# Performance work log

Measured on AMD Instinct MI355X. Metric: run time of the kernel, lower is better.

The kernel has to match this reference:

```python
import jax, jax.numpy as jnp
import numpy as np

EMBED_DIM = 1024
NUM_HEADS = 16
HEAD_DIM = EMBED_DIM // NUM_HEADS
SCALE = 1.0 / float(np.sqrt(HEAD_DIM))


def setup_inputs() -> dict:
    key = jax.random.key(0)
    ks = jax.random.split(key, 5)
    B, S, E = 2, 2048, EMBED_DIM
    x = jax.random.normal(ks[0], (B, S, E), dtype=jnp.float32)
    # nn.Linear-style params (weights stored [out, in] in torch; we keep [in, out] for x @ W)
    w_qkv = jax.random.normal(ks[1], (E, 3 * E), dtype=jnp.float32) / np.sqrt(E)
    b_qkv = jax.random.normal(ks[2], (3 * E,), dtype=jnp.float32) * 0.02
    w_out = jax.random.normal(ks[3], (E, E), dtype=jnp.float32) / np.sqrt(E)
    b_out = jax.random.normal(ks[4], (E,), dtype=jnp.float32) * 0.02
    return {"x": x, "w_qkv": w_qkv, "b_qkv": b_qkv, "w_out": w_out, "b_out": b_out}


def reference(x, w_qkv, b_qkv, w_out, b_out) -> jnp.ndarray:
    B, S, E = x.shape
    H, Dh = NUM_HEADS, HEAD_DIM
    # fused QKV projection
    qkv = x @ w_qkv + b_qkv                                  # [B, S, 3E]
    qkv = qkv.reshape(B, S, 3, H, Dh)
    qkv = jnp.transpose(qkv, (2, 0, 3, 1, 4))                # [3, B, H, S, Dh]
    q, k, v = qkv[0], qkv[1], qkv[2]
    # naive attention (matches _local_attention), is_causal=True
    scores = jnp.einsum('bhqd,bhkd->bhqk', q, k) * SCALE      # [B, H, S, S]
    causal = jnp.triu(jnp.full((S, S), -jnp.inf, dtype=scores.dtype), k=1)
    scores = scores + causal
    attn = jax.nn.softmax(scores, axis=-1)
    out = jnp.einsum('bhqk,bhkd->bhqd', attn, v)              # [B, H, S, Dh]
    out = jnp.transpose(out, (0, 2, 1, 3)).reshape(B, S, E)
    return out @ w_out + b_out
```

## Files before the change

kernel.cpp:

```cpp
#include <hip/hip_runtime.h>
#include <math.h>

static constexpr int Ee  = 1024;
static constexpr int Ss  = 2048;
static constexpr int Bb  = 2;
static constexpr int Hh  = 16;
static constexpr int DHd = 64;
static constexpr int Mm  = Bb * Ss;
static constexpr int Kk  = 1024;

typedef __attribute__((ext_vector_type(8))) short short8;
typedef __attribute__((ext_vector_type(4))) float f32x4;

__device__ __forceinline__ unsigned short f2bf(float f) {
    unsigned u = __float_as_uint(f);
    u += 0x7fffu + ((u >> 16) & 1u);
    return (unsigned short)(u >> 16);
}
__device__ __forceinline__ float bf2f(unsigned short h) {
    return __uint_as_float(((unsigned)h) << 16);
}
__device__ __forceinline__ void hilo(float f, unsigned short& h, unsigned short& l) {
    h = f2bf(f);
    l = f2bf(f - bf2f(h));
}

__global__ __launch_bounds__(256) void cvt_hilo(
    const float* __restrict__ in, unsigned short* __restrict__ hi,
    unsigned short* __restrict__ lo, int n4)
{
    int i = blockIdx.x * 256 + threadIdx.x;
    const int stride = gridDim.x * 256;
    for (; i < n4; i += stride) {
        float4 v = ((const float4*)in)[i];
        ushort4 h, l;
        hilo(v.x, h.x, l.x);
        hilo(v.y, h.y, l.y);
        hilo(v.z, h.z, l.z);
        hilo(v.w, h.w, l.w);
        ((ushort4*)hi)[i] = h;
        ((ushort4*)lo)[i] = l;
    }
}

__global__ __launch_bounds__(256) void cvt_w_t(
    const float* __restrict__ W, unsigned short* __restrict__ hT,
    unsigned short* __restrict__ lT, int N)
{
    __shared__ float tile[64][65];
    const int k0 = blockIdx.x * 64, n0 = blockIdx.y * 64;
    const int t = threadIdx.x;
    const int tr = t >> 4, tc = t & 15;
    #pragma unroll
    for (int i = 0; i < 4; ++i) {
        int k = tr + i * 16;
        float4 v = *(const float4*)&W[(size_t)(k0 + k) * N + n0 + tc * 4];
        tile[k][tc * 4 + 0] = v.x;
        tile[k][tc * 4 + 1] = v.y;
        tile[k][tc * 4 + 2] = v.z;
        tile[k][tc * 4 + 3] = v.w;
    }
    __syncthreads();
    #pragma unroll
    for (int i = 0; i < 4; ++i) {
        int n = tr + i * 16;
        ushort4 h, l;
        hilo(tile[tc * 4 + 0][n], h.x, l.x);
        hilo(tile[tc * 4 + 1][n], h.y, l.y);
        hilo(tile[tc * 4 + 2][n], h.z, l.z);
        hilo(tile[tc * 4 + 3][n], h.w, l.w);
        *(ushort4*)&hT[(size_t)(n0 + n) * Kk + k0 + tc * 4] = h;
        *(ushort4*)&lT[(size_t)(n0 + n) * Kk + k0 + tc * 4] = l;
    }
}

template <int N, bool QKV>
__global__ __launch_bounds__(256) void gemm_bf16x3(
    const unsigned short* __restrict__ Ah, const unsigned short* __restrict__ Al,
    const unsigned short* __restrict__ BhT, const unsigned short* __restrict__ BlT,
    const float* __restrict__ bias, float* __restrict__ O0,
    unsigned short* __restrict__ Qh, unsigned short* __restrict__ Ql,
    unsigned short* __restrict__ Kh, unsigned short* __restrict__ Kl,
    unsigned short* __restrict__ Vh, unsigned short* __restrict__ Vl)
{
    __shared__ __align__(16) unsigned short AsH[128 * 32];
    __shared__ __align__(16) unsigned short AsL[128 * 32];
    __shared__ __align__(16) unsigned short BsH[128 * 32];
    __shared__ __align__(16) unsigned short BsL[128 * 32];

    const int t  = threadIdx.x;
    const int m0 = blockIdx.y * 128, n0 = blockIdx.x * 128;
    const int w  = t >> 6, lane = t & 63;
    const int wr = w >> 1, wc = w & 1;
    const int lr = lane & 15, lk = lane >> 4;

    f32x4 acc[4][4] = {};

    #pragma unroll 1
    for (int k0 = 0; k0 < Kk; k0 += 32) {
        #pragma unroll
        for (int i = 0; i < 2; ++i) {
            const int seg = t + i * 256;
            const int row = seg >> 2, kq = seg & 3;
            const size_t goA = (size_t)(m0 + row) * Kk + k0 + kq * 8;
            const size_t goB = (size_t)(n0 + row) * Kk + k0 + kq * 8;
            const int lo = (i * 256 + (t & ~63)) * 8;
            __builtin_amdgcn_global_load_lds(
                (const __attribute__((address_space(1))) void*)(Ah + goA),
                (__attribute__((address_space(3))) void*)(AsH + lo), 16, 0, 0);
            __builtin_amdgcn_global_load_lds(
                (const __attribute__((address_space(1))) void*)(Al + goA),
                (__attribute__((address_space(3))) void*)(AsL + lo), 16, 0, 0);
            __builtin_amdgcn_global_load_lds(
                (const __attribute__((address_space(1))) void*)(BhT + goB),
                (__attribute__((address_space(3))) void*)(BsH + lo), 16, 0, 0);
            __builtin_amdgcn_global_load_lds(
                (const __attribute__((address_space(1))) void*)(BlT + goB),
                (__attribute__((address_space(3))) void*)(BsL + lo), 16, 0, 0);
        }
        __syncthreads();

        short8 avh[4], avl[4], bvh[4], bvl[4];
        #pragma unroll
        for (int m = 0; m < 4; ++m) {
            const int off = (wr * 64 + m * 16 + lr) * 32 + lk * 8;
            avh[m] = *(const short8*)&AsH[off];
            avl[m] = *(const short8*)&AsL[off];
        }
        #pragma unroll
        for (int n = 0; n < 4; ++n) {
            const int off = (wc * 64 + n * 16 + lr) * 32 + lk * 8;
            bvh[n] = *(const short8*)&BsH[off];
            bvl[n] = *(const short8*)&BsL[off];
        }
        #pragma unroll
        for (int m = 0; m < 4; ++m)
            #pragma unroll
            for (int n = 0; n < 4; ++n) {
                acc[m][n] = __builtin_amdgcn_mfma_f32_16x16x32_bf16(
                    avh[m], bvh[n], acc[m][n], 0, 0, 0);
                acc[m][n] = __builtin_amdgcn_mfma_f32_16x16x32_bf16(
                    avh[m], bvl[n], acc[m][n], 0, 0, 0);
                acc[m][n] = __builtin_amdgcn_mfma_f32_16x16x32_bf16(
                    avl[m], bvh[n], acc[m][n], 0, 0, 0);
            }
        __syncthreads();
    }

    #pragma unroll
    for (int n = 0; n < 4; ++n) {
        const int gcol = n0 + wc * 64 + n * 16 + lr;
        const float bb = bias[gcol];
        if (QKV) {
            const int c  = gcol >> 10;
            const int hd = (gcol >> 6) & 15;
            const int d  = gcol & 63;
            #pragma unroll
            for (int m = 0; m < 4; ++m) {
                #pragma unroll
                for (int r = 0; r < 4; ++r) {
                    const int grow = m0 + wr * 64 + m * 16 + lk * 4 + r;
                    const int b = grow >> 11, s = grow & (Ss - 1);
                    const int bh = b * Hh + hd;
                    const int kv = s & 63;
                    float v = acc[m][n][r] + bb;
                    if (c == 0) v *= 0.125f;
                    unsigned short vh_, vl_;
                    hilo(v, vh_, vl_);
                    size_t off;
                    unsigned short *ph, *pl;
                    if (c == 0) {
                        off = ((size_t)bh * Ss + s) * 64 + d;
                        ph = Qh; pl = Ql;
                    } else if (c == 1) {
                        off = (size_t)bh * 131072 + (size_t)(s >> 6) * 4096 +
                              kv * 64 + (d ^ ((kv & 7) << 3));
                        ph = Kh; pl = Kl;
                    } else {
                        off = (size_t)bh * 131072 + (size_t)(s >> 6) * 4096 +
                              d * 64 + (kv ^ ((d & 7) << 3));
                        ph = Vh; pl = Vl;
                    }
                    ph[off] = vh_;
                    pl[off] = vl_;
                }
            }
        } else {
            #pragma unroll
            for (int m = 0; m < 4; ++m) {
                #pragma unroll
                for (int r = 0; r < 4; ++r) {
                    const int grow = m0 + wr * 64 + m * 16 + lk * 4 + r;
                    O0[(size_t)grow * N + gcol] = acc[m][n][r] + bb;
                }
            }
        }
    }
}

__global__ __launch_bounds__(256, 4) void flash_mfma(
    const unsigned short* __restrict__ Qgh, const unsigned short* __restrict__ Qgl,
    const unsigned short* __restrict__ Kgh, const unsigned short* __restrict__ Kgl,
    const unsigned short* __restrict__ Vgh, const unsigned short* __restrict__ Vgl,
    unsigned short* __restrict__ AOh, unsigned short* __restrict__ AOl)
{
    __shared__ __align__(16) unsigned short Ksh[4096], Ksl[4096];
    __shared__ __align__(16) unsigned short Vsh[4096], Vsl[4096];
    __shared__ __align__(16) unsigned short Ph[4096], Pl[4096];

    const int t    = threadIdx.x;
    const int w    = t >> 6, lane = t & 63;
    const int lr   = lane & 15, g = lane >> 4;
    const int bid  = blockIdx.x;
    const int qt   = 31 - (bid >> 5);
    const int bh   = bid & 31;
    const int b    = bh >> 4, h = bh & 15;
    const int q0   = qt * 64;
    const int wq0  = w * 16;
    const int qloc = wq0 + lr;
    const int qg   = q0 + qloc;

    short8 qbh[2], qbl[2];
    #pragma unroll
    for (int ks = 0; ks < 2; ++ks) {
        const size_t off = ((size_t)bh * Ss + qg) * 64 + ks * 32 + g * 8;
        qbh[ks] = *(const short8*)&Qgh[off];
        qbl[ks] = *(const short8*)&Qgl[off];
    }

    f32x4 o[4] = {};
    float lp = 0.f;

    const int swq = (lr & 7) << 3;

    const int nkt = qt + 1;
    #pragma unroll 1
    for (int kt = 0; kt < nkt; ++kt) {
        const size_t gb = ((size_t)bh * 32 + kt) * 4096;
        #pragma unroll
        for (int i = 0; i < 2; ++i) {
            const int seg = i * 256 + t;
            const int lo = (i * 256 + (t & ~63)) * 8;
            __builtin_amdgcn_global_load_lds(
                (const __attribute__((address_space(1))) void*)(Kgh + gb + seg * 8),
                (__attribute__((address_space(3))) void*)(Ksh + lo), 16, 0, 0);
            __builtin_amdgcn_global_load_lds(
                (const __attribute__((address_space(1))) void*)(Kgl + gb + seg * 8),
                (__attribute__((address_space(3))) void*)(Ksl + lo), 16, 0, 0);
            __builtin_amdgcn_global_load_lds(
                (const __attribute__((address_space(1))) void*)(Vgh + gb + seg * 8),
                (__attribute__((address_space(3))) void*)(Vsh + lo), 16, 0, 0);
            __builtin_amdgcn_global_load_lds(
                (const __attribute__((address_space(1))) void*)(Vgl + gb + seg * 8),
                (__attribute__((address_space(3))) void*)(Vsl + lo), 16, 0, 0);
        }
        __syncthreads();

        f32x4 s[4] = {};
        #pragma unroll
        for (int ks = 0; ks < 2; ++ks) {
            const int d0 = ks * 32 + g * 8;
            #pragma unroll
            for (int n = 0; n < 4; ++n) {
                const int kv = n * 16 + lr;
                const int idx = kv * 64 + (d0 ^ ((kv & 7) << 3));
                const short8 kh = *(const short8*)&Ksh[idx];
                const short8 kl = *(const short8*)&Ksl[idx];
                s[n] = __builtin_amdgcn_mfma_f32_16x16x32_bf16(kh, qbh[ks], s[n], 0, 0, 0);
                s[n] = __builtin_amdgcn_mfma_f32_16x16x32_bf16(kh, qbl[ks], s[n], 0, 0, 0);
                s[n] = __builtin_amdgcn_mfma_f32_16x16x32_bf16(kl, qbh[ks], s[n], 0, 0, 0);
            }
        }

        if (kt == qt) {
            #pragma unroll
            for (int n = 0; n < 4; ++n)
                #pragma unroll
                for (int r = 0; r < 4; ++r) {
                    const int kv = kt * 64 + n * 16 + g * 4 + r;
                    if (kv > qg) s[n][r] = -INFINITY;
                }
        }

        #pragma unroll
        for (int n = 0; n < 4; ++n) {
            const float p0 = exp2f(fmaf(s[n][0], 1.44269504f, -23.0831184f));
            const float p1 = exp2f(fmaf(s[n][1], 1.44269504f, -23.0831184f));
            const float p2 = exp2f(fmaf(s[n][2], 1.44269504f, -23.0831184f));
            const float p3 = exp2f(fmaf(s[n][3], 1.44269504f, -23.0831184f));
            lp += (p0 + p1) + (p2 + p3);
            const unsigned a0 = __float_as_uint(p0), a1 = __float_as_uint(p1);
            const unsigned a2 = __float_as_uint(p2), a3 = __float_as_uint(p3);
            uint2 uh, ul;
            uh.x = (a0 >> 16) | (a1 & 0xffff0000u);
            uh.y = (a2 >> 16) | (a3 & 0xffff0000u);
            const float r0 = p0 - __uint_as_float(a0 & 0xffff0000u);
            const float r1 = p1 - __uint_as_float(a1 & 0xffff0000u);
            const float r2 = p2 - __uint_as_float(a2 & 0xffff0000u);
            const float r3 = p3 - __uint_as_float(a3 & 0xffff0000u);
            ul.x = (__float_as_uint(r0) >> 16) | (__float_as_uint(r1) & 0xffff0000u);
            ul.y = (__float_as_uint(r2) >> 16) | (__float_as_uint(r3) & 0xffff0000u);
            const int kv0 = n * 16 + g * 4;
            const int idx = qloc * 64 + (kv0 ^ swq);
            *(uint2*)&Ph[idx] = uh;
            *(uint2*)&Pl[idx] = ul;
        }

        #pragma unroll
        for (int ks = 0; ks < 2; ++ks) {
            const int kv0 = ks * 32 + g * 8;
            const int pidx = qloc * 64 + (kv0 ^ swq);
            const short8 pah = *(const short8*)&Ph[pidx];
            const short8 pal = *(const short8*)&Pl[pidx];
            #pragma unroll
            for (int df = 0; df < 4; ++df) {
                const int d = df * 16 + lr;
                const int vidx = d * 64 + (kv0 ^ ((d & 7) << 3));
                const short8 vh_ = *(const short8*)&Vsh[vidx];
                const short8 vl_ = *(const short8*)&Vsl[vidx];
                o[df] = __builtin_amdgcn_mfma_f32_16x16x32_bf16(pah, vh_, o[df], 0, 0, 0);
                o[df] = __builtin_amdgcn_mfma_f32_16x16x32_bf16(pah, vl_, o[df], 0, 0, 0);
                o[df] = __builtin_amdgcn_mfma_f32_16x16x32_bf16(pal, vh_, o[df], 0, 0, 0);
            }
        }
        __syncthreads();
    }

    lp += __shfl_xor(lp, 16);
    lp += __shfl_xor(lp, 32);
    float linv[4];
    #pragma unroll
    for (int r = 0; r < 4; ++r)
        linv[r] = 1.f / __shfl(lp, g * 4 + r);

    #pragma unroll
    for (int df = 0; df < 4; ++df) {
        const int col = h * 64 + df * 16 + lr;
        #pragma unroll
        for (int r = 0; r < 4; ++r) {
            const int q = q0 + wq0 + g * 4 + r;
            const size_t off = ((size_t)(b * Ss + q)) * Ee + col;
            const float v = o[df][r] * linv[r];
            const unsigned a = __float_as_uint(v);
            AOh[off] = (unsigned short)(a >> 16);
            const float rr = v - __uint_as_float(a & 0xffff0000u);
            AOl[off] = (unsigned short)(__float_as_uint(rr) >> 16);
        }
    }
}

extern "C" void kernel_launch(void* const* d_in, const int* in_sizes, int n_in,
                              void* d_out, int out_size, void* d_ws, size_t ws_size,
                              hipStream_t stream)
{
    const float* x     = (const float*)d_in[0];
    const float* w_qkv = (const float*)d_in[1];
    const float* b_qkv = (const float*)d_in[2];
    const float* w_out = (const float*)d_in[3];
    const float* b_out = (const float*)d_in[4];
    float* out = (float*)d_out;

    char* wsb = (char*)d_ws;
    const size_t MB = 1024ull * 1024ull;
    unsigned short* Qh = (unsigned short*)(wsb + 0 * MB);
    unsigned short* Ql = (unsigned short*)(wsb + 8 * MB);
    unsigned short* Kh = (unsigned short*)(wsb + 16 * MB);
    unsigned short* Kl = (unsigned short*)(wsb + 24 * MB);
    unsigned short* Vh = (unsigned short*)(wsb + 32 * MB);
    unsigned short* Vl = (unsigned short*)(wsb + 40 * MB);
    unsigned short* Xh = (unsigned short*)(wsb + 48 * MB);
    unsigned short* Xl = (unsigned short*)(wsb + 56 * MB);
    unsigned short* AOh = (unsigned short*)(wsb + 48 * MB);
    unsigned short* AOl = (unsigned short*)(wsb + 56 * MB);
    unsigned short* WqkvhT = (unsigned short*)(wsb + 64 * MB);
    unsigned short* WqkvlT = (unsigned short*)(wsb + 70 * MB);
    unsigned short* WouthT = (unsigned short*)(wsb + 76 * MB);
    unsigned short* WoutlT = (unsigned short*)(wsb + 78 * MB);

    cvt_hilo<<<2048, 256, 0, stream>>>(x, Xh, Xl, Mm * Kk / 4);
    cvt_w_t<<<dim3(Kk / 64, 3072 / 64), 256, 0, stream>>>(w_qkv, WqkvhT, WqkvlT, 3072);
    cvt_w_t<<<dim3(Kk / 64, 1024 / 64), 256, 0, stream>>>(w_out, WouthT, WoutlT, 1024);

    gemm_bf16x3<3072, true><<<dim3(3072 / 128, Mm / 128), 256, 0, stream>>>(
        Xh, Xl, WqkvhT, WqkvlT, b_qkv, nullptr, Qh, Ql, Kh, Kl, Vh, Vl);

    flash_mfma<<<dim3(1024), 256, 0, stream>>>(
        Qh, Ql, Kh, Kl, Vh, Vl, AOh, AOl);

    gemm_bf16x3<1024, false><<<dim3(1024 / 128, Mm / 128), 256, 0, stream>>>(
        AOh, AOl, WouthT, WoutlT, b_out, out,
        nullptr, nullptr, nullptr, nullptr, nullptr, nullptr);
}
```

Measured before the change: 312.4 us.

## Pack hi/lo bf16 operands interleaved with XOR swizzle for GEMM staging

Replaces the separate hi and lo bf16 arrays for X, the weights and the attention output with one packed layout. Each 32-wide k-block stores 32 hi and 32 lo values together per row, with 16-byte groups XOR-swizzled by row. The GEMM now issues two global-to-LDS loads per iteration instead of four into 64-wide tiles, and its fragment reads use the swizzle to avoid LDS bank conflicts. The cost is that the flash kernel now writes its output as scattered 2-byte stores into the swizzled layout, and the converters change their access patterns.

Result: faster. 300.2 us (-3.9%).

```diff
diff --git a/kernel.cpp b/kernel.cpp
--- a/kernel.cpp
+++ b/kernel.cpp
@@ -12,6 +12,7 @@
 typedef __attribute__((ext_vector_type(8))) short short8;
 typedef __attribute__((ext_vector_type(4))) float f32x4;
 
+
 __device__ __forceinline__ unsigned short f2bf(float f) {
     unsigned u = __float_as_uint(f);
     u += 0x7fffu + ((u >> 16) & 1u);
@@ -25,113 +26,119 @@
     l = f2bf(f - bf2f(h));
 }
 
-__global__ __launch_bounds__(256) void cvt_hilo(
-    const float* __restrict__ in, unsigned short* __restrict__ hi,
-    unsigned short* __restrict__ lo, int n4)
+__global__ __launch_bounds__(256) void cvt_x_packed(
+    const float* __restrict__ in, unsigned short* __restrict__ outp)
 {
-    int i = blockIdx.x * 256 + threadIdx.x;
-    const int stride = gridDim.x * 256;
-    for (; i < n4; i += stride) {
-        float4 v = ((const float4*)in)[i];
-        ushort4 h, l;
-        hilo(v.x, h.x, l.x);
-        hilo(v.y, h.y, l.y);
-        hilo(v.z, h.z, l.z);
-        hilo(v.w, h.w, l.w);
-        ((ushort4*)hi)[i] = h;
-        ((ushort4*)lo)[i] = l;
-    }
-}
-
-__global__ __launch_bounds__(256) void cvt_w_t(
-    const float* __restrict__ W, unsigned short* __restrict__ hT,
-    unsigned short* __restrict__ lT, int N)
+    const int i   = blockIdx.x * 256 + threadIdx.x;
+    const int row = i >> 7;
+    const int ki  = i & 127;
+    const int kb  = ki >> 2;
+    const int gl  = ki & 3;
+    const float4 v0 = *(const float4*)&in[(size_t)row * 1024 + ki * 8];
+    const float4 v1 = *(const float4*)&in[(size_t)row * 1024 + ki * 8 + 4];
+    const float f[8] = {v0.x, v0.y, v0.z, v0.w, v1.x, v1.y, v1.z, v1.w};
+    short8 hv, lv;
+    #pragma unroll
+    for (int j = 0; j < 8; ++j) {
+        unsigned short h, l;
+        hilo(f[j], h, l);
+        hv[j] = (short)h;
+        lv[j] = (short)l;
+    }
+    unsigned short* base = outp + (size_t)row * 2048 + kb * 64;
+    const int sw = row & 7;
+    *(short8*)(base + ((gl ^ sw) << 3))       = hv;
+    *(short8*)(base + (((gl | 4) ^ sw) << 3)) = lv;
+}
+
+__global__ __launch_bounds__(256) void cvt_w_packed(
+    const float* __restrict__ W, unsigned short* __restrict__ Wp, int N)
 {
-    __shared__ float tile[64][65];
-    const int k0 = blockIdx.x * 64, n0 = blockIdx.y * 64;
-    const int t = threadIdx.x;
-    const int tr = t >> 4, tc = t & 15;
-    #pragma unroll
-    for (int i = 0; i < 4; ++i) {
-        int k = tr + i * 16;
-        float4 v = *(const float4*)&W[(size_t)(k0 + k) * N + n0 + tc * 4];
-        tile[k][tc * 4 + 0] = v.x;
-        tile[k][tc * 4 + 1] = v.y;
-        tile[k][tc * 4 + 2] = v.z;
-        tile[k][tc * 4 + 3] = v.w;
+    __shared__ float tile[32][65];
+    const int kb = blockIdx.x;
+    const int n0 = blockIdx.y * 64;
+    const int k0 = kb * 32;
+    const int t  = threadIdx.x;
+    {
+        const int kr = t >> 4, nc = t & 15;
+        #pragma unroll
+        for (int i = 0; i < 2; ++i) {
+            const int k = kr + i * 16;
+            float4 v = *(const float4*)&W[(size_t)(k0 + k) * N + n0 + nc * 4];
+            tile[k][nc * 4 + 0] = v.x;
+            tile[k][nc * 4 + 1] = v.y;
+            tile[k][nc * 4 + 2] = v.z;
+            tile[k][nc * 4 + 3] = v.w;
+        }
     }
     __syncthreads();
-    #pragma unroll
-    for (int i = 0; i < 4; ++i) {
-        int n = tr + i * 16;
-        ushort4 h, l;
-        hilo(tile[tc * 4 + 0][n], h.x, l.x);
-        hilo(tile[tc * 4 + 1][n], h.y, l.y);
-        hilo(tile[tc * 4 + 2][n], h.z, l.z);
-        hilo(tile[tc * 4 + 3][n], h.w, l.w);
-        *(ushort4*)&hT[(size_t)(n0 + n) * Kk + k0 + tc * 4] = h;
-        *(ushort4*)&lT[(size_t)(n0 + n) * Kk + k0 + tc * 4] = l;
-    }
+    const int n  = t >> 2;
+    const int gl = t & 3;
+    const int ng = n0 + n;
+    short8 hv, lv;
+    #pragma unroll
+    for (int j = 0; j < 8; ++j) {
+        unsigned short h, l;
+        hilo(tile[gl * 8 + j][n], h, l);
+        hv[j] = (short)h;
+        lv[j] = (short)l;
+    }
+    unsigned short* base = Wp + (size_t)ng * 2048 + kb * 64;
+    const int sw = ng & 7;
+    *(short8*)(base + ((gl ^ sw) << 3))       = hv;
+    *(short8*)(base + (((gl | 4) ^ sw) << 3)) = lv;
 }
 
 template <int N, bool QKV>
 __global__ __launch_bounds__(256) void gemm_bf16x3(
-    const unsigned short* __restrict__ Ah, const unsigned short* __restrict__ Al,
-    const unsigned short* __restrict__ BhT, const unsigned short* __restrict__ BlT,
+    const unsigned short* __restrict__ Ap, const unsigned short* __restrict__ Bp,
     const float* __restrict__ bias, float* __restrict__ O0,
     unsigned short* __restrict__ Qh, unsigned short* __restrict__ Ql,
     unsigned short* __restrict__ Kh, unsigned short* __restrict__ Kl,
     unsigned short* __restrict__ Vh, unsigned short* __restrict__ Vl)
 {
-    __shared__ __align__(16) unsigned short AsH[128 * 32];
-    __shared__ __align__(16) unsigned short AsL[128 * 32];
-    __shared__ __align__(16) unsigned short BsH[128 * 32];
-    __shared__ __align__(16) unsigned short BsL[128 * 32];
+    __shared__ __align__(16) unsigned short As[128 * 64];
+    __shared__ __align__(16) unsigned short Bs[128 * 64];
 
     const int t  = threadIdx.x;
     const int m0 = blockIdx.y * 128, n0 = blockIdx.x * 128;
     const int w  = t >> 6, lane = t & 63;
     const int wr = w >> 1, wc = w & 1;
     const int lr = lane & 15, lk = lane >> 4;
+    const int sw = lr & 7;
 
     f32x4 acc[4][4] = {};
 
     #pragma unroll 1
-    for (int k0 = 0; k0 < Kk; k0 += 32) {
-        #pragma unroll
-        for (int i = 0; i < 2; ++i) {
+    for (int kb = 0; kb < 32; ++kb) {
+        #pragma unroll
+        for (int i = 0; i < 4; ++i) {
             const int seg = t + i * 256;
-            const int row = seg >> 2, kq = seg & 3;
-            const size_t goA = (size_t)(m0 + row) * Kk + k0 + kq * 8;
-            const size_t goB = (size_t)(n0 + row) * Kk + k0 + kq * 8;
+            const int row = seg >> 3, gp = seg & 7;
+            const size_t goA = (size_t)(m0 + row) * 2048 + kb * 64 + gp * 8;
+            const size_t goB = (size_t)(n0 + row) * 2048 + kb * 64 + gp * 8;
             const int lo = (i * 256 + (t & ~63)) * 8;
             __builtin_amdgcn_global_load_lds(
-                (const __attribute__((address_space(1))) void*)(Ah + goA),
-                (__attribute__((address_space(3))) void*)(AsH + lo), 16, 0, 0);
-            __builtin_amdgcn_global_load_lds(
-                (const __attribute__((address_space(1))) void*)(Al + goA),
-                (__attribute__((address_space(3))) void*)(AsL + lo), 16, 0, 0);
-            __builtin_amdgcn_global_load_lds(
-                (const __attribute__((address_space(1))) void*)(BhT + goB),
-                (__attribute__((address_space(3))) void*)(BsH + lo), 16, 0, 0);
-            __builtin_amdgcn_global_load_lds(
-                (const __attribute__((address_space(1))) void*)(BlT + goB),
-                (__attribute__((address_space(3))) void*)(BsL + lo), 16, 0, 0);
+                (const __attribute__((address_space(1))) void*)(Ap + goA),
+                (__attribute__((address_space(3))) void*)(As + lo), 16, 0, 0);
+            __builtin_amdgcn_global_load_lds(
+                (const __attribute__((address_space(1))) void*)(Bp + goB),
+                (__attribute__((address_space(3))) void*)(Bs + lo), 16, 0, 0);
         }
         __syncthreads();
 
         short8 avh[4], avl[4], bvh[4], bvl[4];
         #pragma unroll
         for (int m = 0; m < 4; ++m) {
-            const int off = (wr * 64 + m * 16 + lr) * 32 + lk * 8;
-            avh[m] = *(const short8*)&AsH[off];
-            avl[m] = *(const short8*)&AsL[off];
+            const int rb = (wr * 64 + m * 16 + lr) * 64;
+            avh[m] = *(const short8*)&As[rb + ((lk ^ sw) << 3)];
+            avl[m] = *(const short8*)&As[rb + (((lk | 4) ^ sw) << 3)];
         }
         #pragma unroll
         for (int n = 0; n < 4; ++n) {
-            const int off = (wc * 64 + n * 16 + lr) * 32 + lk * 8;
-            bvh[n] = *(const short8*)&BsH[off];
-            bvl[n] = *(const short8*)&BsL[off];
+            const int rb = (wc * 64 + n * 16 + lr) * 64;
+            bvh[n] = *(const short8*)&Bs[rb + ((lk ^ sw) << 3)];
+            bvl[n] = *(const short8*)&Bs[rb + (((lk | 4) ^ sw) << 3)];
         }
         #pragma unroll
         for (int m = 0; m < 4; ++m)
@@ -202,7 +209,7 @@
     const unsigned short* __restrict__ Qgh, const unsigned short* __restrict__ Qgl,
     const unsigned short* __restrict__ Kgh, const unsigned short* __restrict__ Kgl,
     const unsigned short* __restrict__ Vgh, const unsigned short* __restrict__ Vgl,
-    unsigned short* __restrict__ AOh, unsigned short* __restrict__ AOl)
+    unsigned short* __restrict__ AOp)
 {
     __shared__ __align__(16) unsigned short Ksh[4096], Ksl[4096];
     __shared__ __align__(16) unsigned short Vsh[4096], Vsl[4096];
@@ -230,7 +237,6 @@
 
     f32x4 o[4] = {};
     float lp = 0.f;
-
     const int swq = (lr & 7) << 3;
 
     const int nkt = qt + 1;
@@ -335,16 +341,21 @@
 
     #pragma unroll
     for (int df = 0; df < 4; ++df) {
-        const int col = h * 64 + df * 16 + lr;
+        const int k = h * 64 + df * 16 + lr;
+        const int kb2 = k >> 5, gl = (k >> 3) & 3, el = k & 7;
         #pragma unroll
         for (int r = 0; r < 4; ++r) {
             const int q = q0 + wq0 + g * 4 + r;
-            const size_t off = ((size_t)(b * Ss + q)) * Ee + col;
+            const int m = b * Ss + q;
             const float v = o[df][r] * linv[r];
             const unsigned a = __float_as_uint(v);
-            AOh[off] = (unsigned short)(a >> 16);
+            const unsigned short hh = (unsigned short)(a >> 16);
             const float rr = v - __uint_as_float(a & 0xffff0000u);
-            AOl[off] = (unsigned short)(__float_as_uint(rr) >> 16);
+            const unsigned short ll = (unsigned short)(__float_as_uint(rr) >> 16);
+            unsigned short* bse = AOp + (size_t)m * 2048 + kb2 * 64;
+            const int sw = m & 7;
+            bse[((gl ^ sw) << 3) + el]       = hh;
+            bse[(((gl | 4) ^ sw) << 3) + el] = ll;
         }
     }
 }
@@ -362,32 +373,28 @@
 
     char* wsb = (char*)d_ws;
     const size_t MB = 1024ull * 1024ull;
-    unsigned short* Qh = (unsigned short*)(wsb + 0 * MB);
-    unsigned short* Ql = (unsigned short*)(wsb + 8 * MB);
-    unsigned short* Kh = (unsigned short*)(wsb + 16 * MB);
-    unsigned short* Kl = (unsigned short*)(wsb + 24 * MB);
-    unsigned short* Vh = (unsigned short*)(wsb + 32 * MB);
-    unsigned short* Vl = (unsigned short*)(wsb + 40 * MB);
-    unsigned short* Xh = (unsigned short*)(wsb + 48 * MB);
-    unsigned short* Xl = (unsigned short*)(wsb + 56 * MB);
-    unsigned short* AOh = (unsigned short*)(wsb + 48 * MB);
-    unsigned short* AOl = (unsigned short*)(wsb + 56 * MB);
-    unsigned short* WqkvhT = (unsigned short*)(wsb + 64 * MB);
-    unsigned short* WqkvlT = (unsigned short*)(wsb + 70 * MB);
-    unsigned short* WouthT = (unsigned short*)(wsb + 76 * MB);
-    unsigned short* WoutlT = (unsigned short*)(wsb + 78 * MB);
-
-    cvt_hilo<<<2048, 256, 0, stream>>>(x, Xh, Xl, Mm * Kk / 4);
-    cvt_w_t<<<dim3(Kk / 64, 3072 / 64), 256, 0, stream>>>(w_qkv, WqkvhT, WqkvlT, 3072);
-    cvt_w_t<<<dim3(Kk / 64, 1024 / 64), 256, 0, stream>>>(w_out, WouthT, WoutlT, 1024);
+    unsigned short* Qh  = (unsigned short*)(wsb + 0 * MB);
+    unsigned short* Ql  = (unsigned short*)(wsb + 8 * MB);
+    unsigned short* Kh  = (unsigned short*)(wsb + 16 * MB);
+    unsigned short* Kl  = (unsigned short*)(wsb + 24 * MB);
+    unsigned short* Vh  = (unsigned short*)(wsb + 32 * MB);
+    unsigned short* Vl  = (unsigned short*)(wsb + 40 * MB);
+    unsigned short* Xp  = (unsigned short*)(wsb + 48 * MB);
+    unsigned short* AOp = (unsigned short*)(wsb + 48 * MB);
+    unsigned short* Wqkvp = (unsigned short*)(wsb + 64 * MB);
+    unsigned short* Woutp = (unsigned short*)(wsb + 76 * MB);
+
+    cvt_x_packed<<<2048, 256, 0, stream>>>(x, Xp);
+    cvt_w_packed<<<dim3(32, 3072 / 64), 256, 0, stream>>>(w_qkv, Wqkvp, 3072);
+    cvt_w_packed<<<dim3(32, 1024 / 64), 256, 0, stream>>>(w_out, Woutp, 1024);
 
     gemm_bf16x3<3072, true><<<dim3(3072 / 128, Mm / 128), 256, 0, stream>>>(
-        Xh, Xl, WqkvhT, WqkvlT, b_qkv, nullptr, Qh, Ql, Kh, Kl, Vh, Vl);
+        Xp, Wqkvp, b_qkv, nullptr, Qh, Ql, Kh, Kl, Vh, Vl);
 
     flash_mfma<<<dim3(1024), 256, 0, stream>>>(
-        Qh, Ql, Kh, Kl, Vh, Vl, AOh, AOl);
+        Qh, Ql, Kh, Kl, Vh, Vl, AOp);
 
     gemm_bf16x3<1024, false><<<dim3(1024 / 128, Mm / 128), 256, 0, stream>>>(
-        AOh, AOl, WouthT, WoutlT, b_out, out,
+        AOp, Woutp, b_out, out,
         nullptr, nullptr, nullptr, nullptr, nullptr, nullptr);
 }
```
